# Optimization experiments

Hardware: AMD Instinct MI355X
Metric: run time of the kernel (lower is better)

## Reference

```python
import jax, jax.numpy as jnp
import numpy as np

B = 4096        # batch_size
D = 256         # feature_dim
N = 9000000     # dataset size (state buffer length)
G = 100         # num_groups
ALPHA = 0.5     # alpha_weight
GAMMA = 0.8
RHO = 8.0
LAM = 1.0       # lambada
ETA_P = 0.01
EPS = 1e-14
CLIP = 5.0


def setup_inputs() -> dict:
    key = jax.random.key(0)
    k = jax.random.split(key, 6)
    zis = jax.random.normal(k[0], (B, D), jnp.float32)
    zjs = jax.random.normal(k[1], (B, D), jnp.float32)
    # per-sample learned temperatures, small positive values
    taus_I = 0.01 + 0.2 * jax.random.uniform(k[2], (N,), jnp.float32)
    taus_T = 0.01 + 0.2 * jax.random.uniform(k[3], (N,), jnp.float32)
    group_info_I = jax.random.randint(k[4], (N,), 0, G, dtype=jnp.int32)
    group_info_T = jax.random.randint(k[5], (N,), 0, G, dtype=jnp.int32)
    ids = jnp.arange(B, dtype=jnp.int32)  # unique sample indices
    zeros_N = jnp.zeros((N,), jnp.float32)
    return {
        "zis": zis, "zjs": zjs,
        "s_I": zeros_N, "s_T": zeros_N, "b_I": zeros_N, "b_T": zeros_N,
        "z_I": jnp.zeros((G,), jnp.float32), "z_T": jnp.zeros((G,), jnp.float32),
        "p_I": jnp.ones((G,), jnp.float32) / G, "p_T": jnp.ones((G,), jnp.float32) / G,
        "taus_I": taus_I, "taus_T": taus_T,
        "ids": ids, "group_info_I": group_info_I, "group_info_T": group_info_T,
    }


def _l2norm(x):
    return x / jnp.maximum(jnp.linalg.norm(x, axis=1, keepdims=True), 1e-12)


def reference(zis, zjs, s_I, s_T, b_I, b_T, z_I, z_T, p_I, p_T,
              taus_I, taus_T, ids, group_info_I, group_info_T):
    zis = _l2norm(zis)
    zjs = _l2norm(zjs)
    sim = zis @ zjs.T                                   # [B, B]
    diag = jnp.diagonal(sim)                            # [B]
    mask_neg = 1.0 - jnp.eye(B, dtype=sim.dtype)
    image_diffs = sim - diag[:, None]
    text_diffs = sim - diag[None, :]

    tau_I = taus_I[ids]                                 # [B]
    tau_T = taus_T[ids]
    idt = jax.lax.stop_gradient(image_diffs / tau_I[:, None])
    tdt = jax.lax.stop_gradient(text_diffs / tau_T[None, :])

    # running max state (numerically-stable exp)
    old_b_I = b_I[ids]
    b_I_new = jnp.maximum(jnp.max(idt, axis=1), old_b_I)    # [B]
    old_b_T = b_T[ids]
    b_T_new = jnp.maximum(jnp.max(tdt, axis=0), old_b_T)    # [B]
    b_I = b_I.at[ids].set(b_I_new)
    b_T = b_T.at[ids].set(b_T_new)

    exp_I = jnp.exp(idt - b_I_new[:, None]) * mask_neg
    exp_T = jnp.exp(tdt - b_T_new[None, :]) * mask_neg
    g_I = jnp.sum(exp_I, axis=1)                         # [B]
    g_T = jnp.sum(exp_T, axis=0)                         # [B]

    # EMA of softmax denominators with max-rescaling
    s_I_new = (1.0 - GAMMA) * s_I[ids] * jnp.exp(old_b_I - b_I_new) + GAMMA * g_I
    s_T_new = (1.0 - GAMMA) * s_T[ids] * jnp.exp(old_b_T - b_T_new) + GAMMA * g_T
    s_I = s_I.at[ids].set(s_I_new)
    s_T = s_T.at[ids].set(s_T_new)
    s_I_c = jnp.maximum(s_I_new, EPS)
    s_T_c = jnp.maximum(s_T_new, EPS)

    w_I = exp_I / s_I_c[:, None]
    w_T = exp_T / s_T_c[None, :]

    gid_I = group_info_I[ids]                            # [B]
    gid_T = group_info_T[ids]
    gw_I = G * p_I[gid_I]                                # [B]
    gw_T = G * p_T[gid_T]

    image_loss = jnp.sum(w_I * gw_I[:, None] * image_diffs, axis=1)   # [B]
    text_loss = jnp.sum(w_T * gw_T[None, :] * text_diffs, axis=0)     # [B]
    total_loss = ALPHA * image_loss.mean() + (1.0 - ALPHA) * text_loss.mean()

    # per-group adversarial weight update
    F_I = tau_I * (jnp.log(s_I_c) + b_I_new + RHO)       # [B]
    F_T = tau_T * (jnp.log(s_T_c) + b_T_new + RHO)
    ones_b = jnp.ones((B,), sim.dtype)
    cnt_I = jnp.maximum(jax.ops.segment_sum(ones_b, gid_I, num_segments=G), 1.0)
    cnt_T = jnp.maximum(jax.ops.segment_sum(ones_b, gid_T, num_segments=G), 1.0)
    grad_p_I = jax.ops.segment_sum(F_I, gid_I, num_segments=G) / cnt_I
    grad_p_T = jax.ops.segment_sum(F_T, gid_T, num_segments=G) / cnt_T

    z_I = (1.0 - GAMMA) * z_I + GAMMA * grad_p_I
    z_T = (1.0 - GAMMA) * z_T + GAMMA * grad_p_T
    grad_hp_I = -LAM * jnp.log(p_I + EPS) - LAM
    grad_hp_T = -LAM * jnp.log(p_T + EPS) - LAM
    new_p_I = p_I * jnp.exp(2.0 * ETA_P * jnp.clip(z_I + grad_hp_I, -CLIP, CLIP))
    new_p_T = p_T * jnp.exp(2.0 * ETA_P * jnp.clip(z_T + grad_hp_T, -CLIP, CLIP))
    p_I = new_p_I / new_p_I.sum()
    p_T = new_p_T / new_p_T.sum()

    return total_loss, p_I, p_T
```

## Files before the change

kernel.cpp:

```cpp
#include <hip/hip_runtime.h>
#include <hip/hip_bf16.h>
#include <math.h>

#define BB 4096
#define DD 256
#define GG 100
#define GAMMA_C 0.8f
#define RHO_C 8.0f
#define ALPHA_C 0.5f
#define EPS_C 1e-14f
#define NS2 64

typedef __bf16 bf16x8 __attribute__((ext_vector_type(8)));
typedef float f32x16 __attribute__((ext_vector_type(16)));

__device__ inline int swz32(int r, int k) {
    return ((r >> 5) << 13) | ((k >> 4) << 9) |
           (((((k >> 3) & 1) << 5) | (r & 31)) << 3) | (k & 7);
}

__device__ inline float blockReduceSum(float v, float* lds) {
    for (int o = 32; o > 0; o >>= 1) v += __shfl_down(v, o);
    int lane = threadIdx.x & 63, wid = threadIdx.x >> 6;
    if (lane == 0) lds[wid] = v;
    __syncthreads();
    if (threadIdx.x == 0) {
        float r = lds[0];
        int nw = blockDim.x >> 6;
        for (int w = 1; w < nw; w++) r += lds[w];
        lds[0] = r;
    }
    __syncthreads();
    float r = lds[0];
    __syncthreads();
    return r;
}

__global__ void norm_kernel(const float* __restrict__ zis,
                            const float* __restrict__ zjs,
                            ushort* __restrict__ zhi, ushort* __restrict__ zlo,
                            ushort* __restrict__ whi, ushort* __restrict__ wlo,
                            float* __restrict__ diag, float* __restrict__ acc) {
    __shared__ float lds[8];
    int r = blockIdx.x;
    if (r == 0) { acc[threadIdx.x] = 0.f; acc[threadIdx.x + 256] = 0.f; }
    float zv = zis[r * DD + threadIdx.x];
    float wv = zjs[r * DD + threadIdx.x];
    float sz = blockReduceSum(zv * zv, lds);
    float sw = blockReduceSum(wv * wv, lds);
    float nz = zv * (1.0f / fmaxf(sqrtf(sz), 1e-12f));
    float nw = wv * (1.0f / fmaxf(sqrtf(sw), 1e-12f));
    float dt = blockReduceSum(nz * nw, lds);
    if (threadIdx.x == 0) diag[r] = dt;
    __hip_bfloat16 hz = __float2bfloat16(nz);
    __hip_bfloat16 lz = __float2bfloat16(nz - __bfloat162float(hz));
    __hip_bfloat16 hw = __float2bfloat16(nw);
    __hip_bfloat16 lw = __float2bfloat16(nw - __bfloat162float(hw));
    int si = swz32(r, threadIdx.x);
    zhi[si] = *(ushort*)&hz;
    zlo[si] = *(ushort*)&lz;
    whi[si] = *(ushort*)&hw;
    wlo[si] = *(ushort*)&lw;
}

__global__ void __launch_bounds__(256, 4) fused_tile(const ushort* __restrict__ Ahi,
        const ushort* __restrict__ Alo, const ushort* __restrict__ Bhi,
        const ushort* __restrict__ Blo, const float* __restrict__ diag,
        const float* __restrict__ tausI, const float* __restrict__ tausT,
        const int* __restrict__ ids,
        float* __restrict__ pmR, float* __restrict__ pgR, float* __restrict__ pwR,
        float* __restrict__ pmC, float* __restrict__ pgC, float* __restrict__ pwC) {
    __shared__ float rDiag[128], rITau[128];
    __shared__ float cDiag[128], cITau[128];

    int lane = threadIdx.x & 63;
    int wv = threadIdx.x >> 6;
    int wm = wv >> 1, wn = wv & 1;
    int bm = blockIdx.y * 128, bn = blockIdx.x * 128;
    int h = lane >> 5, cl = lane & 31;

    if (threadIdx.x < 128) {
        int r = bm + threadIdx.x;
        rDiag[threadIdx.x] = diag[r];
        rITau[threadIdx.x] = 1.0f / tausI[ids[r]];
    } else {
        int c = bn + threadIdx.x - 128;
        cDiag[threadIdx.x - 128] = diag[c];
        cITau[threadIdx.x - 128] = 1.0f / tausT[ids[c]];
    }

    int aBlk = (bm >> 5) + wm * 2;
    int bBlk = (bn >> 5) + wn * 2;
    int lofs = lane * 8;

    f32x16 acc[2][2] = {};
#pragma unroll
    for (int s = 0; s < 16; s++) {
        int so = s * 512 + lofs;
        bf16x8 ah[2], al[2], bh[2], bl[2];
#pragma unroll
        for (int t = 0; t < 2; t++) {
            ah[t] = *(const bf16x8*)&Ahi[(aBlk + t) * 8192 + so];
            al[t] = *(const bf16x8*)&Alo[(aBlk + t) * 8192 + so];
            bh[t] = *(const bf16x8*)&Bhi[(bBlk + t) * 8192 + so];
            bl[t] = *(const bf16x8*)&Blo[(bBlk + t) * 8192 + so];
        }
#pragma unroll
        for (int t = 0; t < 2; t++)
#pragma unroll
            for (int u = 0; u < 2; u++) {
                acc[t][u] = __builtin_amdgcn_mfma_f32_32x32x16_bf16(ah[t], bh[u], acc[t][u], 0, 0, 0);
                acc[t][u] = __builtin_amdgcn_mfma_f32_32x32x16_bf16(ah[t], bl[u], acc[t][u], 0, 0, 0);
                acc[t][u] = __builtin_amdgcn_mfma_f32_32x32x16_bf16(al[t], bh[u], acc[t][u], 0, 0, 0);
            }
    }
    __syncthreads();

    float cd[2], cit[2];
    for (int u = 0; u < 2; u++) {
        int clloc = wn * 64 + u * 32 + cl;
        cd[u] = cDiag[clloc];
        cit[u] = cITau[clloc];
    }

    float cbloc[2], cg[2] = {}, cw[2] = {};
    for (int u = 0; u < 2; u++) {
        float m = -INFINITY;
        for (int t = 0; t < 2; t++)
            for (int reg = 0; reg < 16; reg++)
                m = fmaxf(m, acc[t][u][reg]);
        m = fmaxf(m, __shfl_xor(m, 32));
        cbloc[u] = (m - cd[u]) * cit[u];
    }
    for (int t = 0; t < 2; t++)
        for (int u = 0; u < 2; u++) {
            int gc = bn + wn * 64 + u * 32 + cl;
            for (int reg = 0; reg < 16; reg++) {
                int gr = bm + wm * 64 + t * 32 + (reg & 3) + 4 * h + 8 * (reg >> 2);
                float v = acc[t][u][reg];
                bool off = gr != gc;
                float dvT = v - cd[u];
                float eT = off ? __expf(dvT * cit[u] - cbloc[u]) : 0.f;
                cg[u] += eT;
                cw[u] += eT * dvT;
            }
        }
    int stripeC = blockIdx.y * 2 + wm;
    for (int u = 0; u < 2; u++) {
        cg[u] += __shfl_xor(cg[u], 32);
        cw[u] += __shfl_xor(cw[u], 32);
        if (h == 0) {
            size_t o = (size_t)stripeC * BB + bn + wn * 64 + u * 32 + cl;
            pmC[o] = cbloc[u];
            pgC[o] = cg[u];
            pwC[o] = cw[u];
        }
    }

    int stripeR = blockIdx.x * 2 + wn;
    for (int t = 0; t < 2; t++)
        for (int q = 0; q < 4; q++) {
            float rd4[4], rit4[4], bloc[4], rg[4] = {}, rw[4] = {};
            for (int j = 0; j < 4; j++) {
                int rl = wm * 64 + t * 32 + 8 * q + 4 * h + j;
                rd4[j] = rDiag[rl];
                rit4[j] = rITau[rl];
            }
            for (int j = 0; j < 4; j++) {
                float m = fmaxf(acc[t][0][4 * q + j], acc[t][1][4 * q + j]);
                for (int mask = 1; mask <= 16; mask <<= 1)
                    m = fmaxf(m, __shfl_xor(m, mask));
                bloc[j] = (m - rd4[j]) * rit4[j];
            }
            for (int u = 0; u < 2; u++) {
                int gc = bn + wn * 64 + u * 32 + cl;
                for (int j = 0; j < 4; j++) {
                    int gr = bm + wm * 64 + t * 32 + 8 * q + 4 * h + j;
                    float v = acc[t][u][4 * q + j];
                    bool off = gr != gc;
                    float dvI = v - rd4[j];
                    float eI = off ? __expf(dvI * rit4[j] - bloc[j]) : 0.f;
                    rg[j] += eI;
                    rw[j] += eI * dvI;
                }
            }
            for (int j = 0; j < 4; j++)
                for (int mask = 1; mask <= 16; mask <<= 1) {
                    rg[j] += __shfl_xor(rg[j], mask);
                    rw[j] += __shfl_xor(rw[j], mask);
                }
            if (cl == 0) {
                size_t o = (size_t)stripeR * BB + bm + wm * 64 + t * 32 + 8 * q + 4 * h;
                *(float4*)&pmR[o] = make_float4(bloc[0], bloc[1], bloc[2], bloc[3]);
                *(float4*)&pgR[o] = make_float4(rg[0], rg[1], rg[2], rg[3]);
                *(float4*)&pwR[o] = make_float4(rw[0], rw[1], rw[2], rw[3]);
            }
        }
}

__global__ void __launch_bounds__(256) fin_kernel(
        const float* __restrict__ pmR, const float* __restrict__ pgR,
        const float* __restrict__ pwR, const float* __restrict__ pmC,
        const float* __restrict__ pgC, const float* __restrict__ pwC,
        const float* __restrict__ sI, const float* __restrict__ bI,
        const float* __restrict__ tausI, const int* __restrict__ gInfI,
        const float* __restrict__ pI,
        const float* __restrict__ sT, const float* __restrict__ bT,
        const float* __restrict__ tausT, const int* __restrict__ gInfT,
        const float* __restrict__ pT,
        const int* __restrict__ ids, float* __restrict__ acc,
        const float* __restrict__ zI, const float* __restrict__ zT,
        float* __restrict__ out) {
    __shared__ float lds[8];
    __shared__ float binF[GG], binC[GG];
    __shared__ int lastFlag;
    if (threadIdx.x < GG) { binF[threadIdx.x] = 0.f; binC[threadIdx.x] = 0.f; }
    __syncthreads();
    int side = blockIdx.x >> 4;
    int i = (blockIdx.x & 15) * 256 + threadIdx.x;
    const float* pm = side ? pmC : pmR;
    const float* pg = side ? pgC : pgR;
    const float* pw = side ? pwC : pwR;
    const float* sS = side ? sT : sI;
    const float* bS = side ? bT : bI;
    const float* taus = side ? tausT : tausI;
    const int* ginfo = side ? gInfT : gInfI;
    const float* pP = side ? pT : pI;

    int id = ids[i];
    float oldb = bS[id];
    float m = -INFINITY;
    for (int s = 0; s < NS2; s++) m = fmaxf(m, pm[(size_t)s * BB + i]);
    float bfin = fmaxf(m, oldb);
    float g = 0.f, wsum = 0.f;
    for (int s = 0; s < NS2; s++) {
        float f = __expf(pm[(size_t)s * BB + i] - bfin);
        g += pg[(size_t)s * BB + i] * f;
        wsum += pw[(size_t)s * BB + i] * f;
    }
    float tau = taus[id];
    float snew = (1.f - GAMMA_C) * sS[id] * expf(oldb - bfin) + GAMMA_C * g;
    float sc = fmaxf(snew, EPS_C);
    int gid = ginfo[id];
    float gw = (float)GG * pP[gid];
    float loss = gw * wsum / sc;
    float F = tau * (logf(sc) + bfin + RHO_C);
    atomicAdd(&binF[gid], F);
    atomicAdd(&binC[gid], 1.0f);
    float lsum = blockReduceSum(loss, lds);
    if (threadIdx.x == 0) atomicAdd(&acc[side], lsum);
    __syncthreads();
    if (threadIdx.x < GG) {
        atomicAdd(&acc[2 + side * 200 + threadIdx.x], binF[threadIdx.x]);
        atomicAdd(&acc[102 + side * 200 + threadIdx.x], binC[threadIdx.x]);
    }

    __threadfence();
    if (threadIdx.x == 0) {
        int old = atomicAdd((int*)&acc[408], 1);
        lastFlag = (old == 31);
    }
    __syncthreads();
    if (!lastFlag) return;

    int gg = threadIdx.x;
    float npI = 0.f, npT = 0.f;
    if (gg < GG) {
        float cI = __hip_atomic_load(&acc[102 + gg], __ATOMIC_RELAXED, __HIP_MEMORY_SCOPE_AGENT);
        float fI = __hip_atomic_load(&acc[2 + gg], __ATOMIC_RELAXED, __HIP_MEMORY_SCOPE_AGENT);
        float gpI = fI / fmaxf(cI, 1.f);
        float zi = (1.f - GAMMA_C) * zI[gg] + GAMMA_C * gpI;
        float ghpI = -logf(pI[gg] + EPS_C) - 1.f;
        float ti = fminf(fmaxf(zi + ghpI, -5.f), 5.f);
        npI = pI[gg] * expf(0.02f * ti);

        float cT = __hip_atomic_load(&acc[302 + gg], __ATOMIC_RELAXED, __HIP_MEMORY_SCOPE_AGENT);
        float fT = __hip_atomic_load(&acc[202 + gg], __ATOMIC_RELAXED, __HIP_MEMORY_SCOPE_AGENT);
        float gpT = fT / fmaxf(cT, 1.f);
        float zt = (1.f - GAMMA_C) * zT[gg] + GAMMA_C * gpT;
        float ghpT = -logf(pT[gg] + EPS_C) - 1.f;
        float tt = fminf(fmaxf(zt + ghpT, -5.f), 5.f);
        npT = pT[gg] * expf(0.02f * tt);
    }
    float sumI = blockReduceSum(npI, lds);
    float sumT = blockReduceSum(npT, lds);
    if (gg < GG) {
        out[1 + gg] = npI / sumI;
        out[101 + gg] = npT / sumT;
    }
    if (gg == 0) {
        float lI = __hip_atomic_load(&acc[0], __ATOMIC_RELAXED, __HIP_MEMORY_SCOPE_AGENT);
        float lT = __hip_atomic_load(&acc[1], __ATOMIC_RELAXED, __HIP_MEMORY_SCOPE_AGENT);
        out[0] = ALPHA_C * (lI / (float)BB) + (1.f - ALPHA_C) * (lT / (float)BB);
    }
}

extern "C" void kernel_launch(void* const* d_in, const int* in_sizes, int n_in,
                              void* d_out, int out_size, void* d_ws, size_t ws_size,
                              hipStream_t stream) {
    const float* zis   = (const float*)d_in[0];
    const float* zjs   = (const float*)d_in[1];
    const float* s_I   = (const float*)d_in[2];
    const float* s_T   = (const float*)d_in[3];
    const float* b_I   = (const float*)d_in[4];
    const float* b_T   = (const float*)d_in[5];
    const float* z_I   = (const float*)d_in[6];
    const float* z_T   = (const float*)d_in[7];
    const float* p_I   = (const float*)d_in[8];
    const float* p_T   = (const float*)d_in[9];
    const float* tausI = (const float*)d_in[10];
    const float* tausT = (const float*)d_in[11];
    const int*   ids   = (const int*)d_in[12];
    const int*   gInfI = (const int*)d_in[13];
    const int*   gInfT = (const int*)d_in[14];
    float* out = (float*)d_out;

    char* ws = (char*)d_ws;
    ushort* zhi = (ushort*)ws;
    ushort* zlo = zhi + (size_t)BB * DD;
    ushort* whi = zlo + (size_t)BB * DD;
    ushort* wlo = whi + (size_t)BB * DD;
    float* acc  = (float*)(wlo + (size_t)BB * DD);
    float* diag = acc + 512;
    float* pmR  = diag + BB;
    float* pgR  = pmR + (size_t)NS2 * BB;
    float* pwR  = pgR + (size_t)NS2 * BB;
    float* pmC  = pwR + (size_t)NS2 * BB;
    float* pgC  = pmC + (size_t)NS2 * BB;
    float* pwC  = pgC + (size_t)NS2 * BB;

    norm_kernel<<<BB, 256, 0, stream>>>(zis, zjs, zhi, zlo, whi, wlo, diag, acc);
    fused_tile<<<dim3(32, 32), 256, 0, stream>>>(zhi, zlo, whi, wlo, diag,
            tausI, tausT, ids, pmR, pgR, pwR, pmC, pgC, pwC);
    fin_kernel<<<32, 256, 0, stream>>>(pmR, pgR, pwR, pmC, pgC, pwC,
            s_I, b_I, tausI, gInfI, p_I, s_T, b_T, tausT, gInfT, p_T, ids, acc,
            z_I, z_T, out);
}
```

Before: 309.8 us.

## Shrink fused tile to 128x64 with register prefetch and batch norm kernel rows

The similarity tile changes from 128x128 to 128x64 per block, and each wave now owns a 32x64 slab. This doubles the grid to 2048 blocks and gives 128 column partial stripes. The K-loop now prefetches the next step's fragments into registers before issuing the MFMAs, to hide global load latency. The norm kernel handles 32 rows per block with float4 loads and wave shuffles, staging the swizzled bf16 hi/lo tiles in LDS and writing them out coalesced. The cost is more partial-stripe traffic for the final reduction and less B-fragment reuse per wave.

```diff
diff --git a/kernel.cpp b/kernel.cpp
--- a/kernel.cpp
+++ b/kernel.cpp
@@ -9,14 +9,14 @@
 #define RHO_C 8.0f
 #define ALPHA_C 0.5f
 #define EPS_C 1e-14f
-#define NS2 64
+#define NSR 64
+#define NSC 128
 
 typedef __bf16 bf16x8 __attribute__((ext_vector_type(8)));
 typedef float f32x16 __attribute__((ext_vector_type(16)));
 
-__device__ inline int swz32(int r, int k) {
-    return ((r >> 5) << 13) | ((k >> 4) << 9) |
-           (((((k >> 3) & 1) << 5) | (r & 31)) << 3) | (k & 7);
+__device__ inline int swzLoc(int r31, int k) {
+    return ((k >> 4) << 9) | (((((k >> 3) & 1) << 5) | r31) << 3) | (k & 7);
 }
 
 __device__ inline float blockReduceSum(float v, float* lds) {
@@ -36,31 +36,57 @@
     return r;
 }
 
-__global__ void norm_kernel(const float* __restrict__ zis,
+__global__ void __launch_bounds__(256) norm_kernel(const float* __restrict__ zis,
                             const float* __restrict__ zjs,
                             ushort* __restrict__ zhi, ushort* __restrict__ zlo,
                             ushort* __restrict__ whi, ushort* __restrict__ wlo,
                             float* __restrict__ diag, float* __restrict__ acc) {
-    __shared__ float lds[8];
-    int r = blockIdx.x;
-    if (r == 0) { acc[threadIdx.x] = 0.f; acc[threadIdx.x + 256] = 0.f; }
-    float zv = zis[r * DD + threadIdx.x];
-    float wv = zjs[r * DD + threadIdx.x];
-    float sz = blockReduceSum(zv * zv, lds);
-    float sw = blockReduceSum(wv * wv, lds);
-    float nz = zv * (1.0f / fmaxf(sqrtf(sz), 1e-12f));
-    float nw = wv * (1.0f / fmaxf(sqrtf(sw), 1e-12f));
-    float dt = blockReduceSum(nz * nw, lds);
-    if (threadIdx.x == 0) diag[r] = dt;
-    __hip_bfloat16 hz = __float2bfloat16(nz);
-    __hip_bfloat16 lz = __float2bfloat16(nz - __bfloat162float(hz));
-    __hip_bfloat16 hw = __float2bfloat16(nw);
-    __hip_bfloat16 lw = __float2bfloat16(nw - __bfloat162float(hw));
-    int si = swz32(r, threadIdx.x);
-    zhi[si] = *(ushort*)&hz;
-    zlo[si] = *(ushort*)&lz;
-    whi[si] = *(ushort*)&hw;
-    wlo[si] = *(ushort*)&lw;
+    __shared__ ushort st[4][8192];
+    int rb = blockIdx.x;
+    int wv = threadIdx.x >> 6, lane = threadIdx.x & 63;
+    if (rb == 0) { acc[threadIdx.x] = 0.f; acc[threadIdx.x + 256] = 0.f; }
+    for (int rr = 0; rr < 8; rr++) {
+        int r = rb * 32 + wv * 8 + rr;
+        float4 zv = *(const float4*)&zis[r * DD + lane * 4];
+        float4 wv4 = *(const float4*)&zjs[r * DD + lane * 4];
+        float sz = zv.x * zv.x + zv.y * zv.y + zv.z * zv.z + zv.w * zv.w;
+        float sw = wv4.x * wv4.x + wv4.y * wv4.y + wv4.z * wv4.z + wv4.w * wv4.w;
+        float dt = zv.x * wv4.x + zv.y * wv4.y + zv.z * wv4.z + zv.w * wv4.w;
+        for (int mask = 1; mask <= 32; mask <<= 1) {
+            sz += __shfl_xor(sz, mask);
+            sw += __shfl_xor(sw, mask);
+            dt += __shfl_xor(dt, mask);
+        }
+        float iz = 1.0f / fmaxf(sqrtf(sz), 1e-12f);
+        float iw = 1.0f / fmaxf(sqrtf(sw), 1e-12f);
+        if (lane == 0) diag[r] = dt * iz * iw;
+        float nz[4] = {zv.x * iz, zv.y * iz, zv.z * iz, zv.w * iz};
+        float nw[4] = {wv4.x * iw, wv4.y * iw, wv4.z * iw, wv4.w * iw};
+        int r31 = wv * 8 + rr;
+        for (int e = 0; e < 4; e++) {
+            int k = lane * 4 + e;
+            int li = swzLoc(r31, k);
+            __hip_bfloat16 hz = __float2bfloat16(nz[e]);
+            __hip_bfloat16 lz = __float2bfloat16(nz[e] - __bfloat162float(hz));
+            __hip_bfloat16 hw = __float2bfloat16(nw[e]);
+            __hip_bfloat16 lw = __float2bfloat16(nw[e] - __bfloat162float(hw));
+            st[0][li] = *(ushort*)&hz;
+            st[1][li] = *(ushort*)&lz;
+            st[2][li] = *(ushort*)&hw;
+            st[3][li] = *(ushort*)&lw;
+        }
+    }
+    __syncthreads();
+    size_t base = (size_t)rb * 8192;
+    ushort* dsts[4] = {zhi + base, zlo + base, whi + base, wlo + base};
+    for (int a = 0; a < 4; a++) {
+        uint4* d = (uint4*)dsts[a];
+        const uint4* s = (const uint4*)st[a];
+        for (int it = 0; it < 4; it++) {
+            int idx = it * 256 + threadIdx.x;
+            d[idx] = s[idx];
+        }
+    }
 }
 
 __global__ void __launch_bounds__(256, 4) fused_tile(const ushort* __restrict__ Ahi,
@@ -71,131 +97,130 @@
         float* __restrict__ pmR, float* __restrict__ pgR, float* __restrict__ pwR,
         float* __restrict__ pmC, float* __restrict__ pgC, float* __restrict__ pwC) {
     __shared__ float rDiag[128], rITau[128];
-    __shared__ float cDiag[128], cITau[128];
+    __shared__ float cDiag[64], cITau[64];
 
     int lane = threadIdx.x & 63;
     int wv = threadIdx.x >> 6;
-    int wm = wv >> 1, wn = wv & 1;
-    int bm = blockIdx.y * 128, bn = blockIdx.x * 128;
+    int bm = blockIdx.y * 128, bn = blockIdx.x * 64;
     int h = lane >> 5, cl = lane & 31;
 
     if (threadIdx.x < 128) {
         int r = bm + threadIdx.x;
         rDiag[threadIdx.x] = diag[r];
         rITau[threadIdx.x] = 1.0f / tausI[ids[r]];
-    } else {
+    } else if (threadIdx.x < 192) {
         int c = bn + threadIdx.x - 128;
         cDiag[threadIdx.x - 128] = diag[c];
         cITau[threadIdx.x - 128] = 1.0f / tausT[ids[c]];
     }
 
-    int aBlk = (bm >> 5) + wm * 2;
-    int bBlk = (bn >> 5) + wn * 2;
+    int aBase = (blockIdx.y * 4 + wv) * 8192;
+    int b0 = (blockIdx.x * 2) * 8192;
+    int b1 = b0 + 8192;
     int lofs = lane * 8;
 
-    f32x16 acc[2][2] = {};
+    f32x16 acc[2] = {};
+    bf16x8 ah, al, bh0, bl0, bh1, bl1;
+    ah  = *(const bf16x8*)&Ahi[aBase + lofs];
+    al  = *(const bf16x8*)&Alo[aBase + lofs];
+    bh0 = *(const bf16x8*)&Bhi[b0 + lofs];
+    bl0 = *(const bf16x8*)&Blo[b0 + lofs];
+    bh1 = *(const bf16x8*)&Bhi[b1 + lofs];
+    bl1 = *(const bf16x8*)&Blo[b1 + lofs];
 #pragma unroll
     for (int s = 0; s < 16; s++) {
-        int so = s * 512 + lofs;
-        bf16x8 ah[2], al[2], bh[2], bl[2];
-#pragma unroll
-        for (int t = 0; t < 2; t++) {
-            ah[t] = *(const bf16x8*)&Ahi[(aBlk + t) * 8192 + so];
-            al[t] = *(const bf16x8*)&Alo[(aBlk + t) * 8192 + so];
-            bh[t] = *(const bf16x8*)&Bhi[(bBlk + t) * 8192 + so];
-            bl[t] = *(const bf16x8*)&Blo[(bBlk + t) * 8192 + so];
-        }
-#pragma unroll
-        for (int t = 0; t < 2; t++)
-#pragma unroll
-            for (int u = 0; u < 2; u++) {
-                acc[t][u] = __builtin_amdgcn_mfma_f32_32x32x16_bf16(ah[t], bh[u], acc[t][u], 0, 0, 0);
-                acc[t][u] = __builtin_amdgcn_mfma_f32_32x32x16_bf16(ah[t], bl[u], acc[t][u], 0, 0, 0);
-                acc[t][u] = __builtin_amdgcn_mfma_f32_32x32x16_bf16(al[t], bh[u], acc[t][u], 0, 0, 0);
-            }
-    }
-    __syncthreads();
-
-    float cd[2], cit[2];
+        bf16x8 nah, nal, nbh0, nbl0, nbh1, nbl1;
+        if (s < 15) {
+            int so = (s + 1) * 512 + lofs;
+            nah  = *(const bf16x8*)&Ahi[aBase + so];
+            nal  = *(const bf16x8*)&Alo[aBase + so];
+            nbh0 = *(const bf16x8*)&Bhi[b0 + so];
+            nbl0 = *(const bf16x8*)&Blo[b0 + so];
+            nbh1 = *(const bf16x8*)&Bhi[b1 + so];
+            nbl1 = *(const bf16x8*)&Blo[b1 + so];
+        }
+        acc[0] = __builtin_amdgcn_mfma_f32_32x32x16_bf16(ah, bh0, acc[0], 0, 0, 0);
+        acc[0] = __builtin_amdgcn_mfma_f32_32x32x16_bf16(ah, bl0, acc[0], 0, 0, 0);
+        acc[0] = __builtin_amdgcn_mfma_f32_32x32x16_bf16(al, bh0, acc[0], 0, 0, 0);
+        acc[1] = __builtin_amdgcn_mfma_f32_32x32x16_bf16(ah, bh1, acc[1], 0, 0, 0);
+        acc[1] = __builtin_amdgcn_mfma_f32_32x32x16_bf16(ah, bl1, acc[1], 0, 0, 0);
+        acc[1] = __builtin_amdgcn_mfma_f32_32x32x16_bf16(al, bh1, acc[1], 0, 0, 0);
+        ah = nah; al = nal; bh0 = nbh0; bl0 = nbl0; bh1 = nbh1; bl1 = nbl1;
+    }
+    __syncthreads();
+
+    float cd2[2], cit2[2], cbloc[2], cg[2] = {}, cw[2] = {};
     for (int u = 0; u < 2; u++) {
-        int clloc = wn * 64 + u * 32 + cl;
-        cd[u] = cDiag[clloc];
-        cit[u] = cITau[clloc];
-    }
-
-    float cbloc[2], cg[2] = {}, cw[2] = {};
+        int clc = u * 32 + cl;
+        cd2[u] = cDiag[clc];
+        cit2[u] = cITau[clc];
+        float m = -INFINITY;
+        for (int reg = 0; reg < 16; reg++) m = fmaxf(m, acc[u][reg]);
+        m = fmaxf(m, __shfl_xor(m, 32));
+        cbloc[u] = (m - cd2[u]) * cit2[u];
+    }
     for (int u = 0; u < 2; u++) {
-        float m = -INFINITY;
-        for (int t = 0; t < 2; t++)
-            for (int reg = 0; reg < 16; reg++)
-                m = fmaxf(m, acc[t][u][reg]);
-        m = fmaxf(m, __shfl_xor(m, 32));
-        cbloc[u] = (m - cd[u]) * cit[u];
-    }
-    for (int t = 0; t < 2; t++)
-        for (int u = 0; u < 2; u++) {
-            int gc = bn + wn * 64 + u * 32 + cl;
-            for (int reg = 0; reg < 16; reg++) {
-                int gr = bm + wm * 64 + t * 32 + (reg & 3) + 4 * h + 8 * (reg >> 2);
-                float v = acc[t][u][reg];
-                bool off = gr != gc;
-                float dvT = v - cd[u];
-                float eT = off ? __expf(dvT * cit[u] - cbloc[u]) : 0.f;
-                cg[u] += eT;
-                cw[u] += eT * dvT;
-            }
-        }
-    int stripeC = blockIdx.y * 2 + wm;
+        int gc = bn + u * 32 + cl;
+        for (int reg = 0; reg < 16; reg++) {
+            int gr = bm + wv * 32 + (reg & 3) + 4 * h + 8 * (reg >> 2);
+            float v = acc[u][reg];
+            bool off = gr != gc;
+            float dvT = v - cd2[u];
+            float eT = off ? __expf(dvT * cit2[u] - cbloc[u]) : 0.f;
+            cg[u] += eT;
+            cw[u] += eT * dvT;
+        }
+    }
+    int stripeC = blockIdx.y * 4 + wv;
     for (int u = 0; u < 2; u++) {
         cg[u] += __shfl_xor(cg[u], 32);
         cw[u] += __shfl_xor(cw[u], 32);
         if (h == 0) {
-            size_t o = (size_t)stripeC * BB + bn + wn * 64 + u * 32 + cl;
+            size_t o = (size_t)stripeC * BB + bn + u * 32 + cl;
             pmC[o] = cbloc[u];
             pgC[o] = cg[u];
             pwC[o] = cw[u];
         }
     }
 
-    int stripeR = blockIdx.x * 2 + wn;
-    for (int t = 0; t < 2; t++)
-        for (int q = 0; q < 4; q++) {
-            float rd4[4], rit4[4], bloc[4], rg[4] = {}, rw[4] = {};
+    int stripeR = blockIdx.x;
+    for (int q = 0; q < 4; q++) {
+        float rd4[4], rit4[4], bloc[4], rg[4] = {}, rw[4] = {};
+        for (int j = 0; j < 4; j++) {
+            int rl = wv * 32 + 8 * q + 4 * h + j;
+            rd4[j] = rDiag[rl];
+            rit4[j] = rITau[rl];
+        }
+        for (int j = 0; j < 4; j++) {
+            float m = fmaxf(acc[0][4 * q + j], acc[1][4 * q + j]);
+            for (int mask = 1; mask <= 16; mask <<= 1)
+                m = fmaxf(m, __shfl_xor(m, mask));
+            bloc[j] = (m - rd4[j]) * rit4[j];
+        }
+        for (int u = 0; u < 2; u++) {
+            int gc = bn + u * 32 + cl;
             for (int j = 0; j < 4; j++) {
-                int rl = wm * 64 + t * 32 + 8 * q + 4 * h + j;
-                rd4[j] = rDiag[rl];
-                rit4[j] = rITau[rl];
+                int gr = bm + wv * 32 + 8 * q + 4 * h + j;
+                float v = acc[u][4 * q + j];
+                bool off = gr != gc;
+                float dvI = v - rd4[j];
+                float eI = off ? __expf(dvI * rit4[j] - bloc[j]) : 0.f;
+                rg[j] += eI;
+                rw[j] += eI * dvI;
             }
-            for (int j = 0; j < 4; j++) {
-                float m = fmaxf(acc[t][0][4 * q + j], acc[t][1][4 * q + j]);
-                for (int mask = 1; mask <= 16; mask <<= 1)
-                    m = fmaxf(m, __shfl_xor(m, mask));
-                bloc[j] = (m - rd4[j]) * rit4[j];
+        }
+        for (int j = 0; j < 4; j++)
+            for (int mask = 1; mask <= 16; mask <<= 1) {
+                rg[j] += __shfl_xor(rg[j], mask);
+                rw[j] += __shfl_xor(rw[j], mask);
             }
-            for (int u = 0; u < 2; u++) {
-                int gc = bn + wn * 64 + u * 32 + cl;
-                for (int j = 0; j < 4; j++) {
-                    int gr = bm + wm * 64 + t * 32 + 8 * q + 4 * h + j;
-                    float v = acc[t][u][4 * q + j];
-                    bool off = gr != gc;
-                    float dvI = v - rd4[j];
-                    float eI = off ? __expf(dvI * rit4[j] - bloc[j]) : 0.f;
-                    rg[j] += eI;
-                    rw[j] += eI * dvI;
-                }
-            }
-            for (int j = 0; j < 4; j++)
-                for (int mask = 1; mask <= 16; mask <<= 1) {
-                    rg[j] += __shfl_xor(rg[j], mask);
-                    rw[j] += __shfl_xor(rw[j], mask);
-                }
-            if (cl == 0) {
-                size_t o = (size_t)stripeR * BB + bm + wm * 64 + t * 32 + 8 * q + 4 * h;
-                *(float4*)&pmR[o] = make_float4(bloc[0], bloc[1], bloc[2], bloc[3]);
-                *(float4*)&pgR[o] = make_float4(rg[0], rg[1], rg[2], rg[3]);
-                *(float4*)&pwR[o] = make_float4(rw[0], rw[1], rw[2], rw[3]);
-            }
-        }
+        if (cl == 0) {
+            size_t o = (size_t)stripeR * BB + bm + wv * 32 + 8 * q + 4 * h;
+            *(float4*)&pmR[o] = make_float4(bloc[0], bloc[1], bloc[2], bloc[3]);
+            *(float4*)&pgR[o] = make_float4(rg[0], rg[1], rg[2], rg[3]);
+            *(float4*)&pwR[o] = make_float4(rw[0], rw[1], rw[2], rw[3]);
+        }
+    }
 }
 
 __global__ void __launch_bounds__(256) fin_kernel(
@@ -218,6 +243,7 @@
     __syncthreads();
     int side = blockIdx.x >> 4;
     int i = (blockIdx.x & 15) * 256 + threadIdx.x;
+    int ns = side ? NSC : NSR;
     const float* pm = side ? pmC : pmR;
     const float* pg = side ? pgC : pgR;
     const float* pw = side ? pwC : pwR;
@@ -230,10 +256,10 @@
     int id = ids[i];
     float oldb = bS[id];
     float m = -INFINITY;
-    for (int s = 0; s < NS2; s++) m = fmaxf(m, pm[(size_t)s * BB + i]);
+    for (int s = 0; s < ns; s++) m = fmaxf(m, pm[(size_t)s * BB + i]);
     float bfin = fmaxf(m, oldb);
     float g = 0.f, wsum = 0.f;
-    for (int s = 0; s < NS2; s++) {
+    for (int s = 0; s < ns; s++) {
         float f = __expf(pm[(size_t)s * BB + i] - bfin);
         g += pg[(size_t)s * BB + i] * f;
         wsum += pw[(size_t)s * BB + i] * f;
@@ -323,14 +349,14 @@
     float* acc  = (float*)(wlo + (size_t)BB * DD);
     float* diag = acc + 512;
     float* pmR  = diag + BB;
-    float* pgR  = pmR + (size_t)NS2 * BB;
-    float* pwR  = pgR + (size_t)NS2 * BB;
-    float* pmC  = pwR + (size_t)NS2 * BB;
-    float* pgC  = pmC + (size_t)NS2 * BB;
-    float* pwC  = pgC + (size_t)NS2 * BB;
-
-    norm_kernel<<<BB, 256, 0, stream>>>(zis, zjs, zhi, zlo, whi, wlo, diag, acc);
-    fused_tile<<<dim3(32, 32), 256, 0, stream>>>(zhi, zlo, whi, wlo, diag,
+    float* pgR  = pmR + (size_t)NSR * BB;
+    float* pwR  = pgR + (size_t)NSR * BB;
+    float* pmC  = pwR + (size_t)NSR * BB;
+    float* pgC  = pmC + (size_t)NSC * BB;
+    float* pwC  = pgC + (size_t)NSC * BB;
+
+    norm_kernel<<<128, 256, 0, stream>>>(zis, zjs, zhi, zlo, whi, wlo, diag, acc);
+    fused_tile<<<dim3(64, 32), 256, 0, stream>>>(zhi, zlo, whi, wlo, diag,
             tausI, tausT, ids, pmR, pgR, pwR, pmC, pgC, pwC);
     fin_kernel<<<32, 256, 0, stream>>>(pmR, pgR, pwR, pmC, pgC, pwC,
             s_I, b_I, tausI, gInfI, p_I, s_T, b_T, tausT, gInfT, p_T, ids, acc,
```

Result: slower. 325.1 us (+5.0%).
